# Performance work log

Hardware: AMD Instinct MI355X
Metric: run time of the kernel (lower is better)

Reference implementation:

```python
import jax, jax.numpy as jnp
import numpy as np

N = 100000
E = 800000
D_IN = 64
D_OUT = 64
SCALES = (4, 8)


def setup_inputs() -> dict:
    key = jax.random.key(0)
    ks = jax.random.split(key, 8)
    x = jax.random.normal(ks[0], (N, D_IN), dtype=jnp.float32)
    edge_index = jax.random.randint(ks[1], (2, E), 0, N, dtype=jnp.int64)
    s = 1.0 / np.sqrt(D_IN)
    W1 = jax.random.uniform(ks[2], (D_OUT, D_IN), minval=-s, maxval=s, dtype=jnp.float32)
    b1 = jax.random.uniform(ks[3], (D_OUT,), minval=-s, maxval=s, dtype=jnp.float32)
    W2 = jax.random.uniform(ks[4], (D_OUT, D_IN), minval=-s, maxval=s, dtype=jnp.float32)
    b2 = jax.random.uniform(ks[5], (D_OUT,), minval=-s, maxval=s, dtype=jnp.float32)
    sg = 1.0 / np.sqrt(D_OUT * len(SCALES))
    Wg = jax.random.uniform(ks[6], (D_OUT, D_OUT * len(SCALES)), minval=-sg, maxval=sg, dtype=jnp.float32)
    bg = jax.random.uniform(ks[7], (D_OUT,), minval=-sg, maxval=sg, dtype=jnp.float32)
    return {"x": x, "edge_index": edge_index, "W1": W1, "b1": b1,
            "W2": W2, "b2": b2, "Wg": Wg, "bg": bg}


def _gconv(x, src, tgt, W, b):
    # scatter-add neighbor features: agg[src] += x[tgt]
    agg = jax.ops.segment_sum(x[tgt], src, num_segments=N)  # [N, D_IN]
    counts = jax.ops.segment_sum(jnp.ones((src.shape[0], 1), x.dtype), src,
                                 num_segments=N) + 1e-6     # [N, 1]
    agg = agg / counts
    return agg @ W.T + b                                    # [N, D_OUT]


def reference(x, edge_index, W1, b1, W2, b2, Wg, bg):
    k_max = E // N  # = 8
    outs = []
    for scale, (W, b) in zip(SCALES, ((W1, b1), (W2, b2))):
        scale = min(scale, k_max)
        src = edge_index[0, :N * scale]
        tgt = edge_index[1, :N * scale]
        outs.append(_gconv(x, src, tgt, W, b))
    multi = jnp.concatenate(outs, axis=-1)                   # [N, 2*D_OUT]
    gate = jax.nn.sigmoid(multi @ Wg.T + bg)                 # [N, D_OUT]
    fused = gate * outs[0] + (1.0 - gate) * outs[1]
    return fused
```

## Files before the change

### kernel.cpp

```cpp
#include <hip/hip_runtime.h>
#include <hip/hip_bf16.h>

#define N_NODES 100000
#define E_TOTAL 800000
#define E1      400000
#define D       64
#define CAP     32

#define NPB        128
#define NB         ((N_NODES + NPB - 1) / NPB)
#define BSTRIDE    (NPB * CAP)
#define BCAP       1536
#define EPB        4096
#define NBKT_BLKS  ((E_TOTAL + EPB - 1) / EPB)

typedef short s16x8 __attribute__((ext_vector_type(8)));
typedef float f32x4 __attribute__((ext_vector_type(4)));
typedef unsigned u32x4 __attribute__((ext_vector_type(4)));

#define WS_CNT     0
#define WS_ENTRIES (N_NODES)
#define WS_W1B     (WS_ENTRIES + N_NODES * CAP)
#define WS_W2B     (WS_W1B + 2048)
#define WS_WGB     (WS_W2B + 2048)
#define WS_BIAS    (WS_WGB + 4096)
#define WS_CUR     (WS_BIAS + 192)
#define WS_XB      (WS_CUR + 800)
#define WS_NEED_BYTES ((size_t)(WS_XB + (size_t)N_NODES * D / 2) * 4)

#define PREP_CONV_THREADS (2048 + 24)
#define PREP_CONV_BLOCKS  ((PREP_CONV_THREADS + 255) / 256)

#define R_X          (N_NODES * D / 8)
#define XCONV_BLOCKS (R_X / 256)

__device__ __forceinline__ float ldv(const void* p, size_t idx, int fp32)
{
    return fp32 ? ((const float*)p)[idx]
                : __bfloat162float(((const __hip_bfloat16*)p)[idx]);
}

__device__ __forceinline__ void detect2(const int* ei, const unsigned short* xu,
                                        int* s2, int& e64, int& fp32)
{
    if (threadIdx.x == 0) { s2[0] = 0; s2[1] = 0; }
    __syncthreads();
    if (threadIdx.x < 16 && ei[2 * threadIdx.x + 1] != 0) atomicOr(&s2[0], 1);
    { unsigned u = xu[threadIdx.x]; if (((u >> 7) & 0xFF) >= 0x90) atomicOr(&s2[1], 1); }
    __syncthreads();
    e64 = (s2[0] == 0); fp32 = s2[1];
}

__global__ __launch_bounds__(256) void prep_kernel(
    const void* __restrict__ xv, const int* __restrict__ ei,
    const void* __restrict__ W1v, const void* __restrict__ b1v,
    const void* __restrict__ W2v, const void* __restrict__ b2v,
    const void* __restrict__ Wgv, const void* __restrict__ bgv,
    unsigned* __restrict__ ws)
{
    __shared__ int s2[2];
    __shared__ unsigned hist[NB];
    __shared__ unsigned bbase[NB];
    int e64, fp32;
    detect2(ei, (const unsigned short*)xv, s2, e64, fp32);

    if (blockIdx.x < NBKT_BLKS) {
        for (int j = threadIdx.x; j < NB; j += 256) hist[j] = 0;
        __syncthreads();

        const int e0 = blockIdx.x * EPB;
        int srcv[16], tgtv[16];
#pragma unroll
        for (int i = 0; i < 16; ++i) {
            const int e = e0 + i * 256 + threadIdx.x;
            srcv[i] = -1;
            if (e < E_TOTAL) {
                if (e64) {
                    srcv[i] = (int)((const uint2*)ei)[e].x;
                    tgtv[i] = (int)((const uint2*)ei)[E_TOTAL + e].x;
                } else {
                    srcv[i] = ei[e]; tgtv[i] = ei[E_TOTAL + e];
                }
            }
        }
        unsigned recv[16], br[16];
#pragma unroll
        for (int i = 0; i < 16; ++i) {
            const int e = e0 + i * 256 + threadIdx.x;
            br[i] = 0xFFFFFFFFu;
            if (srcv[i] >= 0) {
                const unsigned b = (unsigned)srcv[i] >> 7;
                const unsigned r = atomicAdd(&hist[b], 1u);
                recv[i] = (unsigned)tgtv[i]
                        | ((e < E1) ? (1u << 17) : 0u)
                        | (((unsigned)srcv[i] & (NPB - 1)) << 18);
                br[i] = (b << 16) | r;
            }
        }
        __syncthreads();
        for (int j = threadIdx.x; j < NB; j += 256) {
            const unsigned h = hist[j];
            bbase[j] = h ? atomicAdd(ws + WS_CUR + j, h) : 0u;
        }
        __syncthreads();
#pragma unroll
        for (int i = 0; i < 16; ++i) {
            if (br[i] != 0xFFFFFFFFu) {
                const unsigned b = br[i] >> 16, r = br[i] & 0xFFFFu;
                const unsigned pos = bbase[b] + r;
                if (pos < BCAP)
                    ws[WS_ENTRIES + (size_t)b * BSTRIDE + pos] = recv[i];
            }
        }
        return;
    }

    const int gid = (blockIdx.x - NBKT_BLKS) * 256 + threadIdx.x;
    __hip_bfloat16* W1b = (__hip_bfloat16*)(ws + WS_W1B);
    __hip_bfloat16* W2b = (__hip_bfloat16*)(ws + WS_W2B);
    __hip_bfloat16* Wgb = (__hip_bfloat16*)(ws + WS_WGB);
    float* bias = (float*)(ws + WS_BIAS);

    if (gid < 2048) {
#pragma unroll
        for (int k = 0; k < 8; ++k) {
            const int i = gid * 8 + k;
            if (i < 4096)       W1b[i]        = __float2bfloat16(ldv(W1v, i, fp32));
            else if (i < 8192)  W2b[i - 4096] = __float2bfloat16(ldv(W2v, i - 4096, fp32));
            else                Wgb[i - 8192] = __float2bfloat16(ldv(Wgv, i - 8192, fp32));
        }
    } else if (gid < 2072) {
        const int j = gid - 2048;
#pragma unroll
        for (int k = 0; k < 8; ++k) {
            const int i = j * 8 + k;
            if (i < 64)       bias[i] = ldv(b1v, i, fp32);
            else if (i < 128) bias[i] = ldv(b2v, i - 64, fp32);
            else              bias[i] = ldv(bgv, i - 128, fp32);
        }
    }
}

__global__ __launch_bounds__(256) void csr_kernel(
    const void* __restrict__ xv, unsigned* __restrict__ ws, int use_xb)
{
    __shared__ unsigned cnt_l[NPB];
    __shared__ __align__(16) unsigned ent[NPB * CAP];
    __shared__ int s2[1];

    if (blockIdx.x < NB) {
        const int b  = blockIdx.x;
        const int n0 = b * NPB;
        const int nn = min(NPB, N_NODES - n0);

        if (threadIdx.x < NPB) cnt_l[threadIdx.x] = 0;
        __syncthreads();

        const unsigned C = min(ws[WS_CUR + b], (unsigned)BCAP);
        for (unsigned r = threadIdx.x; r < C; r += 256) {
            const unsigned rec = ws[WS_ENTRIES + (size_t)b * BSTRIDE + r];
            const unsigned sl  = rec >> 18;
            const unsigned p   = atomicAdd(&cnt_l[sl], 1u);
            if (p < CAP)
                ent[sl * CAP + p] = (rec & 0x1FFFFu) | ((rec & (1u << 17)) ? 0x80000000u : 0u);
        }
        __syncthreads();

        const int tot4 = (nn * CAP) / 4;
        u32x4* dst = (u32x4*)(ws + WS_ENTRIES + (size_t)n0 * CAP);
        const u32x4* srcp = (const u32x4*)ent;
        for (int j = threadIdx.x; j < tot4; j += 256) dst[j] = srcp[j];

        if (threadIdx.x < nn) ws[WS_CNT + n0 + threadIdx.x] = cnt_l[threadIdx.x];
        return;
    }

    if (threadIdx.x == 0) s2[0] = 0;
    __syncthreads();
    { unsigned u = ((const unsigned short*)xv)[threadIdx.x];
      if (((u >> 7) & 0xFF) >= 0x90) atomicOr(&s2[0], 1); }
    __syncthreads();
    const int fp32 = s2[0];

    const int gid = (blockIdx.x - NB) * 256 + threadIdx.x;
    if (gid < R_X && use_xb && fp32) {
        __hip_bfloat16* Xb = (__hip_bfloat16*)(ws + WS_XB);
        const f32x4 v0 = ((const f32x4*)xv)[2 * gid];
        const f32x4 v1 = ((const f32x4*)xv)[2 * gid + 1];
        s16x8 o;
#pragma unroll
        for (int j = 0; j < 4; ++j) {
            o[j]     = (short)__bfloat16_as_ushort(__float2bfloat16(v0[j]));
            o[4 + j] = (short)__bfloat16_as_ushort(__float2bfloat16(v1[j]));
        }
        *(s16x8*)(Xb + (size_t)gid * 8) = o;
    }
}

__global__ __launch_bounds__(256) void fused_kernel(
    const unsigned* __restrict__ ws, const void* __restrict__ xv,
    void* __restrict__ outv, int use_xb)
{
    __shared__ __align__(16) __hip_bfloat16 sS[16][136];
    __shared__ __align__(16) __hip_bfloat16 sO[16][136];
    __shared__ int s2d[2];

    if (threadIdx.x == 0) s2d[0] = 0;
    __syncthreads();
    { unsigned u = ((const unsigned short*)xv)[threadIdx.x];
      if (((u >> 7) & 0xFF) >= 0x90) atomicOr(&s2d[0], 1); }
    __syncthreads();
    const int fp32 = s2d[0];

    const int w    = threadIdx.x >> 6;
    const int lane = threadIdx.x & 63;
    const int base = blockIdx.x * 16;

    const int direct_f32 = (fp32 && !use_xb);
    const char* xb = (use_xb && fp32) ? (const char*)(ws + WS_XB) : (const char*)xv;
    const float* xf = (const float*)xv;

    unsigned eraw[4], entv[4], degr[4]; int degc[4];
#pragma unroll
    for (int i = 0; i < 4; ++i) {
        const int n = base + w * 4 + i;
        degr[i] = ws[WS_CNT + n];
        eraw[i] = (lane < CAP) ? ws[WS_ENTRIES + (size_t)n * CAP + lane] : 0u;
    }
#pragma unroll
    for (int i = 0; i < 4; ++i) {
        degc[i] = (int)min(degr[i], (unsigned)CAP);
        entv[i] = (lane < degc[i]) ? eraw[i] : 0u;
    }

    const int half = lane >> 5;
    const int cc   = lane & 31;

    if (!direct_f32) {
        int c1[4];
#pragma unroll
        for (int i = 0; i < 4; ++i)
            c1[i] = (int)__popcll(__ballot(entv[i] & 0x80000000u));

        float s1x[4], s1y[4], s2x[4], s2y[4];
#pragma unroll
        for (int i = 0; i < 4; ++i) { s1x[i] = s1y[i] = s2x[i] = s2y[i] = 0.f; }

        int rmax = 0;
#pragma unroll
        for (int i = 0; i < 4; ++i) rmax = max(rmax, (degc[i] + 1) >> 1);
        rmax = (rmax + 3) & ~3;

#pragma unroll 4
        for (int r = 0; r < rmax; ++r) {
#pragma unroll
            for (int i = 0; i < 4; ++i) {
                const int j = 2 * r + half;
                unsigned en = __shfl(entv[i], j);
                en = (j < degc[i]) ? en : 0u;
                unsigned u = *(const unsigned*)(xb + ((size_t)(en & 0x7FFFFFFFu) << 7)
                                                   + ((unsigned)cc << 2));
                u = (j < degc[i]) ? u : 0u;
                const float fx = __uint_as_float(u << 16);
                const float fy = __uint_as_float(u & 0xFFFF0000u);
                const float fl = (en & 0x80000000u) ? 1.f : 0.f;
                s2x[i] += fx; s2y[i] += fy;
                s1x[i] = fmaf(fl, fx, s1x[i]); s1y[i] = fmaf(fl, fy, s1y[i]);
            }
        }

#pragma unroll
        for (int i = 0; i < 4; ++i) {
            const int nl = w * 4 + i;
            float a = s1x[i], b = s1y[i], c = s2x[i], d = s2y[i];
            a += __shfl_xor(a, 32); b += __shfl_xor(b, 32);
            c += __shfl_xor(c, 32); d += __shfl_xor(d, 32);
            const float inv1 = 1.0f / ((float)c1[i] + 1e-6f);
            const float inv2 = 1.0f / ((float)degr[i] + 1e-6f);
            if (lane < 32) {
                const __hip_bfloat162 p1 = __float22bfloat162_rn({a * inv1, b * inv1});
                const __hip_bfloat162 p2 = __float22bfloat162_rn({c * inv2, d * inv2});
                *(__hip_bfloat162*)&sS[nl][2 * cc]      = p1;
                *(__hip_bfloat162*)&sS[nl][64 + 2 * cc] = p2;
            }
        }
    } else {
#pragma unroll
        for (int i = 0; i < 4; ++i) {
            const int nl = w * 4 + i;
            const int c1 = (int)__popcll(__ballot(entv[i] & 0x80000000u));
            float s1x = 0.f, s2x = 0.f;
            for (int j = 0; j < degc[i]; ++j) {
                const unsigned en = __builtin_amdgcn_readlane(entv[i], j);
                const float v = xf[(size_t)(en & 0x7FFFFFFFu) * D + lane];
                s2x += v;
                if (en & 0x80000000u) s1x += v;
            }
            const float inv1 = 1.0f / ((float)c1 + 1e-6f);
            const float inv2 = 1.0f / ((float)degr[i] + 1e-6f);
            sS[nl][lane]      = __float2bfloat16(s1x * inv1);
            sS[nl][64 + lane] = __float2bfloat16(s2x * inv2);
        }
    }
    __syncthreads();

    const int m = lane & 15;
    const int q = lane >> 4;
    const int nd = w * 16 + m;

    const s16x8* W1b = (const s16x8*)(ws + WS_W1B);
    const s16x8* W2b = (const s16x8*)(ws + WS_W2B);
    const s16x8* Wgb = (const s16x8*)(ws + WS_WGB);
    const float* bias = (const float*)(ws + WS_BIAS);

    const s16x8 a1c0 = *(const s16x8*)&sS[m][q * 8];
    const s16x8 a1c1 = *(const s16x8*)&sS[m][32 + q * 8];
    const s16x8 a2c0 = *(const s16x8*)&sS[m][64 + q * 8];
    const s16x8 a2c1 = *(const s16x8*)&sS[m][96 + q * 8];

    f32x4 z = {0.f, 0.f, 0.f, 0.f};
    z = __builtin_amdgcn_mfma_f32_16x16x32_bf16(a1c0, W1b[nd * 8 + q],     z, 0, 0, 0);
    z = __builtin_amdgcn_mfma_f32_16x16x32_bf16(a1c1, W1b[nd * 8 + 4 + q], z, 0, 0, 0);
    f32x4 y = {0.f, 0.f, 0.f, 0.f};
    y = __builtin_amdgcn_mfma_f32_16x16x32_bf16(a2c0, W2b[nd * 8 + q],     y, 0, 0, 0);
    y = __builtin_amdgcn_mfma_f32_16x16x32_bf16(a2c1, W2b[nd * 8 + 4 + q], y, 0, 0, 0);
    const float bb1 = bias[nd], bb2 = bias[64 + nd];
#pragma unroll
    for (int r = 0; r < 4; ++r) { z[r] += bb1; y[r] += bb2; }

#pragma unroll
    for (int r = 0; r < 4; ++r) {
        sO[q * 4 + r][nd]      = __float2bfloat16(z[r]);
        sO[q * 4 + r][64 + nd] = __float2bfloat16(y[r]);
    }
    __syncthreads();

    s16x8 ga[4];
#pragma unroll
    for (int c = 0; c < 4; ++c)
        ga[c] = *(const s16x8*)&sO[m][c * 32 + q * 8];

    f32x4 g4 = {0.f, 0.f, 0.f, 0.f};
#pragma unroll
    for (int c = 0; c < 4; ++c)
        g4 = __builtin_amdgcn_mfma_f32_16x16x32_bf16(ga[c], Wgb[nd * 16 + c * 4 + q], g4, 0, 0, 0);
    const float bbg = bias[128 + nd];

#pragma unroll
    for (int r = 0; r < 4; ++r) {
        const float g = 1.0f / (1.0f + __expf(-(g4[r] + bbg)));
        const float v = g * z[r] + (1.0f - g) * y[r];
        const size_t node = (size_t)(base + q * 4 + r);
        if (fp32) ((float*)outv)[node * 64 + nd] = v;
        else      ((__hip_bfloat16*)outv)[node * 64 + nd] = __float2bfloat16(v);
    }
}

extern "C" void kernel_launch(void* const* d_in, const int* in_sizes, int n_in,
                              void* d_out, int out_size, void* d_ws, size_t ws_size,
                              hipStream_t stream)
{
    const void* x  = d_in[0];
    const int*  ei = (const int*)d_in[1];
    unsigned* ws = (unsigned*)d_ws;

    const int use_xb = (ws_size >= WS_NEED_BYTES) ? 1 : 0;

    hipMemsetAsync(ws + WS_CUR, 0, 800 * sizeof(unsigned), stream);
    prep_kernel<<<NBKT_BLKS + PREP_CONV_BLOCKS, 256, 0, stream>>>(
        x, ei, d_in[2], d_in[3], d_in[4], d_in[5], d_in[6], d_in[7], ws);
    csr_kernel<<<NB + XCONV_BLOCKS, 256, 0, stream>>>(x, ws, use_xb);
    fused_kernel<<<N_NODES / 16, 256, 0, stream>>>(ws, x, d_out, use_xb);
}
```

Before: 150.8 us.

## Drop bf16 x conversion, gather fp32 directly, sort neighbor lists by scale

Removes the pre-pass that converted x to a bf16 copy in the workspace; the fused kernel now gathers fp32 rows directly, two floats per lane, and a half-wave covers a full row. The CSR build now orders each node's neighbors with scale-1 edges first and packs the scale-1 count into the count word, so the flag bit and ballot-popcount are replaced by a simple index compare. The prep kernel uses 512-thread blocks with half the edges per block. The trade is twice the bytes per gather in exchange for skipping a full 25.6MB read plus 12.8MB write conversion pass, and the CSR kernel gains an extra counting pass through shared memory.

```diff
diff --git a/kernel.cpp b/kernel.cpp
--- a/kernel.cpp
+++ b/kernel.cpp
@@ -11,8 +11,10 @@
 #define NB         ((N_NODES + NPB - 1) / NPB)
 #define BSTRIDE    (NPB * CAP)
 #define BCAP       1536
-#define EPB        4096
+#define EPB        2048
 #define NBKT_BLKS  ((E_TOTAL + EPB - 1) / EPB)
+#define PREP_TPB   512
+#define EPT        (EPB / PREP_TPB)
 
 typedef short s16x8 __attribute__((ext_vector_type(8)));
 typedef float f32x4 __attribute__((ext_vector_type(4)));
@@ -25,14 +27,8 @@
 #define WS_WGB     (WS_W2B + 2048)
 #define WS_BIAS    (WS_WGB + 4096)
 #define WS_CUR     (WS_BIAS + 192)
-#define WS_XB      (WS_CUR + 800)
-#define WS_NEED_BYTES ((size_t)(WS_XB + (size_t)N_NODES * D / 2) * 4)
-
-#define PREP_CONV_THREADS (2048 + 24)
-#define PREP_CONV_BLOCKS  ((PREP_CONV_THREADS + 255) / 256)
-
-#define R_X          (N_NODES * D / 8)
-#define XCONV_BLOCKS (R_X / 256)
+
+#define PREP_CONV_BLOCKS 5
 
 __device__ __forceinline__ float ldv(const void* p, size_t idx, int fp32)
 {
@@ -51,7 +47,7 @@
     e64 = (s2[0] == 0); fp32 = s2[1];
 }
 
-__global__ __launch_bounds__(256) void prep_kernel(
+__global__ __launch_bounds__(512) void prep_kernel(
     const void* __restrict__ xv, const int* __restrict__ ei,
     const void* __restrict__ W1v, const void* __restrict__ b1v,
     const void* __restrict__ W2v, const void* __restrict__ b2v,
@@ -65,14 +61,14 @@
     detect2(ei, (const unsigned short*)xv, s2, e64, fp32);
 
     if (blockIdx.x < NBKT_BLKS) {
-        for (int j = threadIdx.x; j < NB; j += 256) hist[j] = 0;
+        for (int j = threadIdx.x; j < NB; j += PREP_TPB) hist[j] = 0;
         __syncthreads();
 
         const int e0 = blockIdx.x * EPB;
-        int srcv[16], tgtv[16];
-#pragma unroll
-        for (int i = 0; i < 16; ++i) {
-            const int e = e0 + i * 256 + threadIdx.x;
+        int srcv[EPT], tgtv[EPT];
+#pragma unroll
+        for (int i = 0; i < EPT; ++i) {
+            const int e = e0 + i * PREP_TPB + threadIdx.x;
             srcv[i] = -1;
             if (e < E_TOTAL) {
                 if (e64) {
@@ -83,28 +79,28 @@
                 }
             }
         }
-        unsigned recv[16], br[16];
-#pragma unroll
-        for (int i = 0; i < 16; ++i) {
-            const int e = e0 + i * 256 + threadIdx.x;
+        unsigned recv[EPT], br[EPT];
+#pragma unroll
+        for (int i = 0; i < EPT; ++i) {
+            const int e = e0 + i * PREP_TPB + threadIdx.x;
             br[i] = 0xFFFFFFFFu;
             if (srcv[i] >= 0) {
                 const unsigned b = (unsigned)srcv[i] >> 7;
                 const unsigned r = atomicAdd(&hist[b], 1u);
                 recv[i] = (unsigned)tgtv[i]
-                        | ((e < E1) ? (1u << 17) : 0u)
+                        | ((e < E1) ? 0x20000u : 0u)
                         | (((unsigned)srcv[i] & (NPB - 1)) << 18);
                 br[i] = (b << 16) | r;
             }
         }
         __syncthreads();
-        for (int j = threadIdx.x; j < NB; j += 256) {
+        for (int j = threadIdx.x; j < NB; j += PREP_TPB) {
             const unsigned h = hist[j];
             bbase[j] = h ? atomicAdd(ws + WS_CUR + j, h) : 0u;
         }
         __syncthreads();
 #pragma unroll
-        for (int i = 0; i < 16; ++i) {
+        for (int i = 0; i < EPT; ++i) {
             if (br[i] != 0xFFFFFFFFu) {
                 const unsigned b = br[i] >> 16, r = br[i] & 0xFFFFu;
                 const unsigned pos = bbase[b] + r;
@@ -115,7 +111,7 @@
         return;
     }
 
-    const int gid = (blockIdx.x - NBKT_BLKS) * 256 + threadIdx.x;
+    const int gid = (blockIdx.x - NBKT_BLKS) * PREP_TPB + threadIdx.x;
     __hip_bfloat16* W1b = (__hip_bfloat16*)(ws + WS_W1B);
     __hip_bfloat16* W2b = (__hip_bfloat16*)(ws + WS_W2B);
     __hip_bfloat16* Wgb = (__hip_bfloat16*)(ws + WS_WGB);
@@ -141,65 +137,63 @@
     }
 }
 
-__global__ __launch_bounds__(256) void csr_kernel(
-    const void* __restrict__ xv, unsigned* __restrict__ ws, int use_xb)
-{
-    __shared__ unsigned cnt_l[NPB];
+__global__ __launch_bounds__(256) void csr_kernel(unsigned* __restrict__ ws)
+{
+    __shared__ unsigned rec_s[BCAP];
     __shared__ __align__(16) unsigned ent[NPB * CAP];
-    __shared__ int s2[1];
-
-    if (blockIdx.x < NB) {
-        const int b  = blockIdx.x;
-        const int n0 = b * NPB;
-        const int nn = min(NPB, N_NODES - n0);
-
-        if (threadIdx.x < NPB) cnt_l[threadIdx.x] = 0;
-        __syncthreads();
-
-        const unsigned C = min(ws[WS_CUR + b], (unsigned)BCAP);
-        for (unsigned r = threadIdx.x; r < C; r += 256) {
-            const unsigned rec = ws[WS_ENTRIES + (size_t)b * BSTRIDE + r];
-            const unsigned sl  = rec >> 18;
-            const unsigned p   = atomicAdd(&cnt_l[sl], 1u);
-            if (p < CAP)
-                ent[sl * CAP + p] = (rec & 0x1FFFFu) | ((rec & (1u << 17)) ? 0x80000000u : 0u);
-        }
-        __syncthreads();
-
-        const int tot4 = (nn * CAP) / 4;
-        u32x4* dst = (u32x4*)(ws + WS_ENTRIES + (size_t)n0 * CAP);
-        const u32x4* srcp = (const u32x4*)ent;
-        for (int j = threadIdx.x; j < tot4; j += 256) dst[j] = srcp[j];
-
-        if (threadIdx.x < nn) ws[WS_CNT + n0 + threadIdx.x] = cnt_l[threadIdx.x];
-        return;
-    }
-
-    if (threadIdx.x == 0) s2[0] = 0;
-    __syncthreads();
-    { unsigned u = ((const unsigned short*)xv)[threadIdx.x];
-      if (((u >> 7) & 0xFF) >= 0x90) atomicOr(&s2[0], 1); }
-    __syncthreads();
-    const int fp32 = s2[0];
-
-    const int gid = (blockIdx.x - NB) * 256 + threadIdx.x;
-    if (gid < R_X && use_xb && fp32) {
-        __hip_bfloat16* Xb = (__hip_bfloat16*)(ws + WS_XB);
-        const f32x4 v0 = ((const f32x4*)xv)[2 * gid];
-        const f32x4 v1 = ((const f32x4*)xv)[2 * gid + 1];
-        s16x8 o;
-#pragma unroll
-        for (int j = 0; j < 4; ++j) {
-            o[j]     = (short)__bfloat16_as_ushort(__float2bfloat16(v0[j]));
-            o[4 + j] = (short)__bfloat16_as_ushort(__float2bfloat16(v1[j]));
-        }
-        *(s16x8*)(Xb + (size_t)gid * 8) = o;
+    __shared__ unsigned n1c[NPB], ctc[NPB], a1[NPB], a2[NPB];
+
+    const int b  = blockIdx.x;
+    const int n0 = b * NPB;
+    const int nn = min(NPB, N_NODES - n0);
+
+    for (int j = threadIdx.x; j < NPB; j += 256) { n1c[j] = 0; ctc[j] = 0; }
+    {
+        const u32x4 z = {0u, 0u, 0u, 0u};
+        for (int j = threadIdx.x; j < NPB * CAP / 4; j += 256) ((u32x4*)ent)[j] = z;
+    }
+    const unsigned C = min(ws[WS_CUR + b], (unsigned)BCAP);
+    for (unsigned r = threadIdx.x; r < C; r += 256)
+        rec_s[r] = ws[WS_ENTRIES + (size_t)b * BSTRIDE + r];
+    __syncthreads();
+
+    for (unsigned r = threadIdx.x; r < C; r += 256) {
+        const unsigned rec = rec_s[r];
+        const unsigned sl  = rec >> 18;
+        atomicAdd(&ctc[sl], 1u);
+        if (rec & 0x20000u) atomicAdd(&n1c[sl], 1u);
+    }
+    __syncthreads();
+    for (int j = threadIdx.x; j < NPB; j += 256) {
+        a1[j] = 0u;
+        a2[j] = min(n1c[j], (unsigned)CAP);
+    }
+    __syncthreads();
+    for (unsigned r = threadIdx.x; r < C; r += 256) {
+        const unsigned rec = rec_s[r];
+        const unsigned sl  = rec >> 18;
+        unsigned p;
+        if (rec & 0x20000u) p = atomicAdd(&a1[sl], 1u);
+        else                p = atomicAdd(&a2[sl], 1u);
+        if (p < CAP) ent[sl * CAP + p] = rec & 0x1FFFFu;
+    }
+    __syncthreads();
+
+    const int tot4 = (nn * CAP) / 4;
+    u32x4* dst = (u32x4*)(ws + WS_ENTRIES + (size_t)n0 * CAP);
+    const u32x4* srcp = (const u32x4*)ent;
+    for (int j = threadIdx.x; j < tot4; j += 256) dst[j] = srcp[j];
+
+    if (threadIdx.x < nn) {
+        const unsigned ct = min(ctc[threadIdx.x], 0xFFFFu);
+        const unsigned p1 = min(n1c[threadIdx.x], (unsigned)CAP);
+        ws[WS_CNT + n0 + threadIdx.x] = ct | (p1 << 16);
     }
 }
 
 __global__ __launch_bounds__(256) void fused_kernel(
     const unsigned* __restrict__ ws, const void* __restrict__ xv,
-    void* __restrict__ outv, int use_xb)
+    void* __restrict__ outv)
 {
     __shared__ __align__(16) __hip_bfloat16 sS[16][136];
     __shared__ __align__(16) __hip_bfloat16 sO[16][136];
@@ -216,90 +210,84 @@
     const int lane = threadIdx.x & 63;
     const int base = blockIdx.x * 16;
 
-    const int direct_f32 = (fp32 && !use_xb);
-    const char* xb = (use_xb && fp32) ? (const char*)(ws + WS_XB) : (const char*)xv;
-    const float* xf = (const float*)xv;
-
-    unsigned eraw[4], entv[4], degr[4]; int degc[4];
+    unsigned entv[4], cw[4];
 #pragma unroll
     for (int i = 0; i < 4; ++i) {
         const int n = base + w * 4 + i;
-        degr[i] = ws[WS_CNT + n];
-        eraw[i] = (lane < CAP) ? ws[WS_ENTRIES + (size_t)n * CAP + lane] : 0u;
-    }
+        cw[i]   = ws[WS_CNT + n];
+        entv[i] = ws[WS_ENTRIES + (size_t)n * CAP + (lane & 31)];
+    }
+    int degc[4], p1c[4]; unsigned degt[4];
 #pragma unroll
     for (int i = 0; i < 4; ++i) {
-        degc[i] = (int)min(degr[i], (unsigned)CAP);
-        entv[i] = (lane < degc[i]) ? eraw[i] : 0u;
+        degt[i] = cw[i] & 0xFFFFu;
+        p1c[i]  = (int)(cw[i] >> 16);
+        degc[i] = (int)min(degt[i], (unsigned)CAP);
     }
 
     const int half = lane >> 5;
     const int cc   = lane & 31;
 
-    if (!direct_f32) {
-        int c1[4];
-#pragma unroll
-        for (int i = 0; i < 4; ++i)
-            c1[i] = (int)__popcll(__ballot(entv[i] & 0x80000000u));
-
-        float s1x[4], s1y[4], s2x[4], s2y[4];
-#pragma unroll
-        for (int i = 0; i < 4; ++i) { s1x[i] = s1y[i] = s2x[i] = s2y[i] = 0.f; }
-
-        int rmax = 0;
-#pragma unroll
-        for (int i = 0; i < 4; ++i) rmax = max(rmax, (degc[i] + 1) >> 1);
-        rmax = (rmax + 3) & ~3;
-
+    float s1x[4], s1y[4], s2x[4], s2y[4];
+#pragma unroll
+    for (int i = 0; i < 4; ++i) { s1x[i] = s1y[i] = s2x[i] = s2y[i] = 0.f; }
+
+    int rmax = 0;
+#pragma unroll
+    for (int i = 0; i < 4; ++i) rmax = max(rmax, (degc[i] + 1) >> 1);
+    rmax = (rmax + 3) & ~3;
+
+    if (fp32) {
+        const char* xb = (const char*)xv;
+        const unsigned ccb = (unsigned)cc << 3;
 #pragma unroll 4
         for (int r = 0; r < rmax; ++r) {
 #pragma unroll
             for (int i = 0; i < 4; ++i) {
                 const int j = 2 * r + half;
-                unsigned en = __shfl(entv[i], j);
-                en = (j < degc[i]) ? en : 0u;
-                unsigned u = *(const unsigned*)(xb + ((size_t)(en & 0x7FFFFFFFu) << 7)
-                                                   + ((unsigned)cc << 2));
+                const unsigned en = (unsigned)__shfl((int)entv[i], j);
+                const uint2 u = *(const uint2*)(xb + (size_t)((en << 8) + ccb));
+                const bool val = j < degc[i];
+                const float fx = val ? __uint_as_float(u.x) : 0.f;
+                const float fy = val ? __uint_as_float(u.y) : 0.f;
+                const float fl = (j < p1c[i]) ? 1.f : 0.f;
+                s2x[i] += fx; s2y[i] += fy;
+                s1x[i] = fmaf(fl, fx, s1x[i]); s1y[i] = fmaf(fl, fy, s1y[i]);
+            }
+        }
+    } else {
+        const char* xb = (const char*)xv;
+        const unsigned ccb = (unsigned)cc << 2;
+#pragma unroll 4
+        for (int r = 0; r < rmax; ++r) {
+#pragma unroll
+            for (int i = 0; i < 4; ++i) {
+                const int j = 2 * r + half;
+                const unsigned en = (unsigned)__shfl((int)entv[i], j);
+                unsigned u = *(const unsigned*)(xb + (size_t)((en << 7) + ccb));
                 u = (j < degc[i]) ? u : 0u;
                 const float fx = __uint_as_float(u << 16);
                 const float fy = __uint_as_float(u & 0xFFFF0000u);
-                const float fl = (en & 0x80000000u) ? 1.f : 0.f;
+                const float fl = (j < p1c[i]) ? 1.f : 0.f;
                 s2x[i] += fx; s2y[i] += fy;
                 s1x[i] = fmaf(fl, fx, s1x[i]); s1y[i] = fmaf(fl, fy, s1y[i]);
             }
         }
-
-#pragma unroll
-        for (int i = 0; i < 4; ++i) {
-            const int nl = w * 4 + i;
-            float a = s1x[i], b = s1y[i], c = s2x[i], d = s2y[i];
-            a += __shfl_xor(a, 32); b += __shfl_xor(b, 32);
-            c += __shfl_xor(c, 32); d += __shfl_xor(d, 32);
-            const float inv1 = 1.0f / ((float)c1[i] + 1e-6f);
-            const float inv2 = 1.0f / ((float)degr[i] + 1e-6f);
-            if (lane < 32) {
-                const __hip_bfloat162 p1 = __float22bfloat162_rn({a * inv1, b * inv1});
-                const __hip_bfloat162 p2 = __float22bfloat162_rn({c * inv2, d * inv2});
-                *(__hip_bfloat162*)&sS[nl][2 * cc]      = p1;
-                *(__hip_bfloat162*)&sS[nl][64 + 2 * cc] = p2;
-            }
-        }
-    } else {
-#pragma unroll
-        for (int i = 0; i < 4; ++i) {
-            const int nl = w * 4 + i;
-            const int c1 = (int)__popcll(__ballot(entv[i] & 0x80000000u));
-            float s1x = 0.f, s2x = 0.f;
-            for (int j = 0; j < degc[i]; ++j) {
-                const unsigned en = __builtin_amdgcn_readlane(entv[i], j);
-                const float v = xf[(size_t)(en & 0x7FFFFFFFu) * D + lane];
-                s2x += v;
-                if (en & 0x80000000u) s1x += v;
-            }
-            const float inv1 = 1.0f / ((float)c1 + 1e-6f);
-            const float inv2 = 1.0f / ((float)degr[i] + 1e-6f);
-            sS[nl][lane]      = __float2bfloat16(s1x * inv1);
-            sS[nl][64 + lane] = __float2bfloat16(s2x * inv2);
+    }
+
+#pragma unroll
+    for (int i = 0; i < 4; ++i) {
+        const int nl = w * 4 + i;
+        float a = s1x[i], b = s1y[i], c = s2x[i], d = s2y[i];
+        a += __shfl_xor(a, 32); b += __shfl_xor(b, 32);
+        c += __shfl_xor(c, 32); d += __shfl_xor(d, 32);
+        const float inv1 = 1.0f / ((float)p1c[i] + 1e-6f);
+        const float inv2 = 1.0f / ((float)degt[i] + 1e-6f);
+        if (lane < 32) {
+            const __hip_bfloat162 p1 = __float22bfloat162_rn({a * inv1, b * inv1});
+            const __hip_bfloat162 p2 = __float22bfloat162_rn({c * inv2, d * inv2});
+            *(__hip_bfloat162*)&sS[nl][2 * cc]      = p1;
+            *(__hip_bfloat162*)&sS[nl][64 + 2 * cc] = p2;
         }
     }
     __syncthreads();
@@ -364,11 +352,9 @@
     const int*  ei = (const int*)d_in[1];
     unsigned* ws = (unsigned*)d_ws;
 
-    const int use_xb = (ws_size >= WS_NEED_BYTES) ? 1 : 0;
-
     hipMemsetAsync(ws + WS_CUR, 0, 800 * sizeof(unsigned), stream);
-    prep_kernel<<<NBKT_BLKS + PREP_CONV_BLOCKS, 256, 0, stream>>>(
+    prep_kernel<<<NBKT_BLKS + PREP_CONV_BLOCKS, PREP_TPB, 0, stream>>>(
         x, ei, d_in[2], d_in[3], d_in[4], d_in[5], d_in[6], d_in[7], ws);
-    csr_kernel<<<NB + XCONV_BLOCKS, 256, 0, stream>>>(x, ws, use_xb);
-    fused_kernel<<<N_NODES / 16, 256, 0, stream>>>(ws, x, d_out, use_xb);
-}
+    csr_kernel<<<NB, 256, 0, stream>>>(ws);
+    fused_kernel<<<N_NODES / 16, 256, 0, stream>>>(ws, x, d_out);
+}
```

Result: slower. 165.8 us (+10.0%).
